# Optimization experiments

Measured on AMD Instinct MI355X. Metric: run time of the kernel, lower is better.

The kernel has to match this reference:

```python
import jax, jax.numpy as jnp
import numpy as np

N, C, H, W = 4, 64, 64, 64
EPS = 1e-5


def setup_inputs() -> dict:
    key = jax.random.key(0)
    ks = jax.random.split(key, 8)
    f = lambda k, s: jax.random.normal(k, s, dtype=jnp.float32)
    return {
        "low_feats": f(ks[0], (N, C, H, W)),
        "heat0": f(ks[1], (N, C, H, W)),
        "heat1": f(ks[2], (N, C, H, W)),
        # f_query: 1x1 conv + BN(gamma,beta) + ReLU
        "Wq": f(ks[3], (C, C)) * 0.05, "bq": jnp.zeros((C,), jnp.float32),
        "gq": jnp.ones((C,), jnp.float32), "betaq": jnp.zeros((C,), jnp.float32),
        # f_key: 1x1 conv + BN + ReLU
        "Wk": f(ks[4], (C, C)) * 0.05, "bk": jnp.zeros((C,), jnp.float32),
        "gk": jnp.ones((C,), jnp.float32), "betak": jnp.zeros((C,), jnp.float32),
        # f_value: plain 1x1 conv
        "Wv": f(ks[5], (C, C)) * 0.05, "bv": jnp.zeros((C,), jnp.float32),
    }


def _conv1x1(x, Wc, bc):
    # [N,C,H,W] -> [N,O,H,W]
    return jnp.einsum("oc,nchw->nohw", Wc, x) + bc[None, :, None, None]


def _conv_bn_relu(x, Wc, bc, g, beta):
    y = _conv1x1(x, Wc, bc)
    mu = y.mean(axis=(0, 2, 3), keepdims=True)      # batch-stat BN (train mode)
    var = y.var(axis=(0, 2, 3), keepdims=True)
    y = (y - mu) * jax.lax.rsqrt(var + EPS)
    y = y * g[None, :, None, None] + beta[None, :, None, None]
    return jax.nn.relu(y)


def reference(low_feats, heat0, heat1, Wq, bq, gq, betaq, Wk, bk, gk, betak, Wv, bv):
    n, c, h, w = low_feats.shape
    hw = h * w
    query = _conv_bn_relu(low_feats, Wq, bq, gq, betaq).reshape(n, c, hw).transpose(0, 2, 1)  # [N,HW,C]
    keym = _conv_bn_relu(low_feats, Wk, bk, gk, betak).reshape(n, c, hw)                      # [N,C,HW]
    value = _conv1x1(low_feats, Wv, bv).reshape(n, c, hw).transpose(0, 2, 1)                  # [N,HW,C]
    sim = jax.nn.softmax(jnp.einsum("nqc,nck->nqk", query, keym), axis=-1)                    # [N,HW,HW]
    # dual gated value paths share the softmax map: sim@vI + sim@vC == sim@(vI+vC)
    gate = (heat0 + heat1).reshape(n, c, hw).transpose(0, 2, 1)                               # [N,HW,C]
    gated_v = gate * value
    ctx = jnp.einsum("nqk,nkc->nqc", sim, gated_v)                                            # [N,HW,C]
    return ctx.transpose(0, 2, 1).reshape(n, c, h, w)
```

## Files before the change

### kernel.cpp

```cpp
#include <hip/hip_runtime.h>

#define NB 4
#define CC 64
#define HW 4096
#define NT (NB*HW)
#define EPSV 1e-5f
#define LOG2E 1.4426950408889634f
#define THRV 8.0f

typedef _Float16 f16;
typedef _Float16 half4 __attribute__((ext_vector_type(4)));
typedef _Float16 half8 __attribute__((ext_vector_type(8)));
typedef float   float4v __attribute__((ext_vector_type(4)));

#define NELEM ((size_t)NB*HW*CC)
#define NSLOT 128

#define PART_OFF 512
#define TEN_OFF  264192

__global__ __launch_bounds__(256)
void conv2_kernel(const float* __restrict__ x,
                  const float* __restrict__ h0, const float* __restrict__ h1,
                  const float* __restrict__ Wq, const float* __restrict__ bq,
                  const float* __restrict__ Wk, const float* __restrict__ bk,
                  const float* __restrict__ Wv, const float* __restrict__ bv,
                  float* __restrict__ ws,
                  f16* __restrict__ q, f16* __restrict__ k, f16* __restrict__ gv)
{
    __shared__ float Wl[3][16*CC];
    __shared__ float xs[CC][128];
    const int t    = threadIdx.x;
    const int n    = blockIdx.y;
    const int z    = blockIdx.z;
    const int px0  = blockIdx.x * 128;
    const int lane = t & 63;
    const int grp  = t >> 6;
    const int ocl  = grp * 4;
    const int oc0  = z*16 + ocl;

    ((float4*)Wl[0])[t] = ((const float4*)(Wq + (size_t)z*16*CC))[t];
    ((float4*)Wl[1])[t] = ((const float4*)(Wk + (size_t)z*16*CC))[t];
    ((float4*)Wl[2])[t] = ((const float4*)(Wv + (size_t)z*16*CC))[t];
    for (int i = t; i < CC*32; i += 256) {
        int ic = i >> 5, c4 = i & 31;
        ((float4*)&xs[ic][0])[c4] =
            ((const float4*)(x + ((size_t)n*CC + ic)*HW + px0))[c4];
    }
    __syncthreads();

    float aq[4][2], ak[4][2], av[4][2];
    #pragma unroll
    for (int j = 0; j < 4; ++j) {
        aq[j][0] = aq[j][1] = bq[oc0+j];
        ak[j][0] = ak[j][1] = bk[oc0+j];
        av[j][0] = av[j][1] = bv[oc0+j];
    }

    for (int ic = 0; ic < CC; ic += 4) {
        float2 xv0 = *(float2*)&xs[ic  ][lane*2];
        float2 xv1 = *(float2*)&xs[ic+1][lane*2];
        float2 xv2 = *(float2*)&xs[ic+2][lane*2];
        float2 xv3 = *(float2*)&xs[ic+3][lane*2];
        #pragma unroll
        for (int j = 0; j < 4; ++j) {
            const int row = (ocl+j)*CC + ic;
            float4 wq = *(const float4*)&Wl[0][row];
            float4 wk = *(const float4*)&Wl[1][row];
            float4 wv = *(const float4*)&Wl[2][row];
            aq[j][0] = fmaf(wq.x,xv0.x, fmaf(wq.y,xv1.x, fmaf(wq.z,xv2.x, fmaf(wq.w,xv3.x, aq[j][0]))));
            aq[j][1] = fmaf(wq.x,xv0.y, fmaf(wq.y,xv1.y, fmaf(wq.z,xv2.y, fmaf(wq.w,xv3.y, aq[j][1]))));
            ak[j][0] = fmaf(wk.x,xv0.x, fmaf(wk.y,xv1.x, fmaf(wk.z,xv2.x, fmaf(wk.w,xv3.x, ak[j][0]))));
            ak[j][1] = fmaf(wk.x,xv0.y, fmaf(wk.y,xv1.y, fmaf(wk.z,xv2.y, fmaf(wk.w,xv3.y, ak[j][1]))));
            av[j][0] = fmaf(wv.x,xv0.x, fmaf(wv.y,xv1.x, fmaf(wv.z,xv2.x, fmaf(wv.w,xv3.x, av[j][0]))));
            av[j][1] = fmaf(wv.x,xv0.y, fmaf(wv.y,xv1.y, fmaf(wv.z,xv2.y, fmaf(wv.w,xv3.y, av[j][1]))));
        }
    }

    const int px = px0 + lane*2;
    const size_t base = ((size_t)n*HW + px)*CC + oc0;
    half4 vq0, vq1, vk0, vk1;
    #pragma unroll
    for (int j = 0; j < 4; ++j) {
        vq0[j] = (f16)aq[j][0]; vq1[j] = (f16)aq[j][1];
        vk0[j] = (f16)ak[j][0]; vk1[j] = (f16)ak[j][1];
    }
    *(half4*)&q[base]      = vq0;  *(half4*)&q[base + CC] = vq1;
    *(half4*)&k[base]      = vk0;  *(half4*)&k[base + CC] = vk1;

    #pragma unroll
    for (int j = 0; j < 4; ++j) {
        size_t gi = ((size_t)n*CC + oc0 + j)*HW + px;
        f16 g0 = (f16)((h0[gi]   + h1[gi]  ) * av[j][0]);
        f16 g1 = (f16)((h0[gi+1] + h1[gi+1]) * av[j][1]);
        gv[gi]   = g0;
        gv[gi+1] = g1;
    }

    float* slot = ws + PART_OFF + (size_t)(n*(HW/128) + blockIdx.x)*256;
    #pragma unroll
    for (int j = 0; j < 4; ++j) {
        float v0 = aq[j][0] + aq[j][1];
        float v1 = aq[j][0]*aq[j][0] + aq[j][1]*aq[j][1];
        float v2 = ak[j][0] + ak[j][1];
        float v3 = ak[j][0]*ak[j][0] + ak[j][1]*ak[j][1];
        #pragma unroll
        for (int off = 32; off > 0; off >>= 1) {
            v0 += __shfl_down(v0, off);
            v1 += __shfl_down(v1, off);
            v2 += __shfl_down(v2, off);
            v3 += __shfl_down(v3, off);
        }
        if (lane == 0) {
            slot[      oc0 + j] = v0;
            slot[ 64 + oc0 + j] = v1;
            slot[128 + oc0 + j] = v2;
            slot[192 + oc0 + j] = v3;
        }
    }
}

__global__ __launch_bounds__(256)
void apply_kernel(f16* __restrict__ q, f16* __restrict__ k,
                  const float* __restrict__ ws,
                  const float* __restrict__ gq, const float* __restrict__ betaq,
                  const float* __restrict__ gk, const float* __restrict__ betak)
{
    __shared__ float tot[128];
    __shared__ float sc[CC], sh[CC];
    const int t = threadIdx.x;
    const int tens = blockIdx.y;

    if (t < 128) {
        const float* base = ws + PART_OFF + tens*128 + t;
        float acc = 0.0f;
        #pragma unroll 8
        for (int s = 0; s < NSLOT; ++s) acc += base[(size_t)s*256];
        tot[t] = acc;
    }
    __syncthreads();
    if (t < 64) {
        float mean = tot[t] * (1.0f / NT);
        float var  = tot[64 + t] * (1.0f / NT) - mean*mean;
        if (tens == 0) {
            float s = gq[t] * rsqrtf(var + EPSV);
            sc[t] = s;  sh[t] = betaq[t] - mean*s;
        } else {
            float s = gk[t] * rsqrtf(var + EPSV);
            sc[t] = s * LOG2E;  sh[t] = (betak[t] - mean*s) * LOG2E;
        }
    }
    __syncthreads();

    f16* p = tens ? k : q;
    const size_t e0 = ((size_t)blockIdx.x * 256 + t) * 16;
    const int c0 = (int)(e0 & 63);

    half8 v0 = *(half8*)&p[e0], v1 = *(half8*)&p[e0 + 8];
    half8 o0, o1;
    #pragma unroll
    for (int j = 0; j < 8; ++j) {
        o0[j] = (f16)fmaxf(fmaf(sc[c0+j],   (float)v0[j], sh[c0+j]),   0.0f);
        o1[j] = (f16)fmaxf(fmaf(sc[c0+8+j], (float)v1[j], sh[c0+8+j]), 0.0f);
    }
    *(half8*)&p[e0]     = o0;
    *(half8*)&p[e0 + 8] = o1;
}

__global__ __launch_bounds__(512, 4)
void attn_kernel(const f16* __restrict__ q, const f16* __restrict__ k,
                 const f16* __restrict__ gv, float* __restrict__ out)
{
    __shared__ alignas(16) char SM[65536];
    f16 (* const Ks)[2][2048]    = reinterpret_cast<f16(*)[2][2048]>(SM);
    f16 (* const GVs)[2][2048]   = reinterpret_cast<f16(*)[2][2048]>(SM + 32768);
    float (* const Obuf)[4][256] = reinterpret_cast<float(*)[4][256]>(SM);
    float (* const MLbuf)[8][16] = reinterpret_cast<float(*)[8][16]>(SM + 32768);

    const int t    = threadIdx.x;
    const int n    = blockIdx.y;
    const int w    = t >> 6;
    const int lane = t & 63;
    const int m16  = lane & 15;
    const int kb   = lane >> 4;
    const int qi   = w >> 2;
    const int si   = w & 3;
    const int q0g  = blockIdx.x * 32 + qi * 16;

    half8 qf0, qf1;
    {
        const size_t qb = ((size_t)n*HW + q0g + m16)*CC + kb*8;
        qf0 = *(const half8*)&q[qb];
        qf1 = *(const half8*)&q[qb + 32];
    }

    const f16* kn  = k  + (size_t)n*HW*CC;
    const f16* gvn = gv + (size_t)n*CC*HW;

    const int rl  = lane >> 3, cl  = lane & 7;
    const int chl = lane >> 2, kcl = lane & 3;
    const int    srcK = rl*CC + cl*8;
    const int    dstK = rl*CC + ((cl ^ rl) * 8);
    const size_t srcG = (size_t)chl*HW + kcl*8;
    const int    dstG = chl*32 + ((kcl ^ (chl & 3)) * 8);

    const int kt00 = si * 1024;

    const int swzk = (m16 & 7) << 3;
    const int swzg = (m16 & 3) << 3;
    const int e0k  = (kb*8)      ^ swzk;
    const int e1k  = (kb*8 + 32) ^ swzk;

    half8 stg[4];

#define STAGE_LOAD(IT) do {                                                   \
    const int kt_ = kt00 + (IT)*32;                                           \
    if (qi == 0) {                                                            \
        const f16* s_ = kn + (size_t)kt_*CC + srcK;                           \
        stg[0] = *(const half8*)(s_);                                         \
        stg[1] = *(const half8*)(s_ +  8*CC);                                 \
        stg[2] = *(const half8*)(s_ + 16*CC);                                 \
        stg[3] = *(const half8*)(s_ + 24*CC);                                 \
    } else {                                                                  \
        const f16* s_ = gvn + srcG + kt_;                                     \
        stg[0] = *(const half8*)(s_);                                         \
        stg[1] = *(const half8*)(s_ + (size_t)16*HW);                         \
        stg[2] = *(const half8*)(s_ + (size_t)32*HW);                         \
        stg[3] = *(const half8*)(s_ + (size_t)48*HW);                         \
    }                                                                         \
} while (0)

#define STAGE_WRITE(BUF) do {                                                 \
    if (qi == 0) {                                                            \
        f16* d_ = &Ks[si][BUF][dstK];                                         \
        *(half8*)(d_)        = stg[0];                                        \
        *(half8*)(d_ +  512) = stg[1];                                        \
        *(half8*)(d_ + 1024) = stg[2];                                        \
        *(half8*)(d_ + 1536) = stg[3];                                        \
    } else {                                                                  \
        f16* d_ = &GVs[si][BUF][dstG];                                        \
        *(half8*)(d_)        = stg[0];                                        \
        *(half8*)(d_ +  512) = stg[1];                                        \
        *(half8*)(d_ + 1024) = stg[2];                                        \
        *(half8*)(d_ + 1536) = stg[3];                                        \
    }                                                                         \
} while (0)

    float4v accO[4];
    #pragma unroll
    for (int ct = 0; ct < 4; ++ct) accO[ct] = (float4v){0.f,0.f,0.f,0.f};
    float accL = 0.0f;
    float mreg = -INFINITY;

#define COMPUTE(CUR) do {                                                     \
    const f16* Kb_ = &Ks[si][CUR][0];                                         \
    const f16* Gb_ = &GVs[si][CUR][0];                                        \
    half8 kh00_ = *(const half8*)&Kb_[ m16*CC       + e0k];                   \
    half8 kh01_ = *(const half8*)&Kb_[ m16*CC       + e1k];                   \
    half8 kh10_ = *(const half8*)&Kb_[(m16+16)*CC   + e0k];                   \
    half8 kh11_ = *(const half8*)&Kb_[(m16+16)*CC   + e1k];                   \
    float4v s0_ = {0.f,0.f,0.f,0.f}, s1_ = {0.f,0.f,0.f,0.f};                 \
    s0_ = __builtin_amdgcn_mfma_f32_16x16x32_f16(kh00_, qf0, s0_, 0,0,0);     \
    s0_ = __builtin_amdgcn_mfma_f32_16x16x32_f16(kh01_, qf1, s0_, 0,0,0);     \
    s1_ = __builtin_amdgcn_mfma_f32_16x16x32_f16(kh10_, qf0, s1_, 0,0,0);     \
    s1_ = __builtin_amdgcn_mfma_f32_16x16x32_f16(kh11_, qf1, s1_, 0,0,0);     \
    float v_ = fmaxf(fmaxf(fmaxf(s0_[0],s0_[1]), fmaxf(s0_[2],s0_[3])),       \
                     fmaxf(fmaxf(s1_[0],s1_[1]), fmaxf(s1_[2],s1_[3])));      \
    v_ = fmaxf(v_, __shfl_xor(v_, 16));                                       \
    v_ = fmaxf(v_, __shfl_xor(v_, 32));                                       \
    if (__any(v_ > mreg + THRV)) {                                            \
        float mn_ = fmaxf(mreg, v_);                                          \
        float al_ = exp2f(mreg - mn_);                                        \
        mreg = mn_;  accL *= al_;                                             \
        _Pragma("unroll") for (int ct_ = 0; ct_ < 4; ++ct_) {                 \
            accO[ct_][0]*=al_; accO[ct_][1]*=al_;                             \
            accO[ct_][2]*=al_; accO[ct_][3]*=al_;                             \
        }                                                                     \
    }                                                                         \
    float p0_=exp2f(s0_[0]-mreg), p1_=exp2f(s0_[1]-mreg);                     \
    float p2_=exp2f(s0_[2]-mreg), p3_=exp2f(s0_[3]-mreg);                     \
    float p4_=exp2f(s1_[0]-mreg), p5_=exp2f(s1_[1]-mreg);                     \
    float p6_=exp2f(s1_[2]-mreg), p7_=exp2f(s1_[3]-mreg);                     \
    accL += ((p0_+p1_)+(p2_+p3_)) + ((p4_+p5_)+(p6_+p7_));                    \
    half4 pfa_, pfb_;                                                         \
    pfa_[0]=(f16)p0_; pfa_[1]=(f16)p1_; pfa_[2]=(f16)p2_; pfa_[3]=(f16)p3_;   \
    pfb_[0]=(f16)p4_; pfb_[1]=(f16)p5_; pfb_[2]=(f16)p6_; pfb_[3]=(f16)p7_;   \
    _Pragma("unroll") for (int ct_ = 0; ct_ < 4; ++ct_) {                     \
        const int gb_ = (ct_*16 + m16)*32;                                    \
        half4 g0_ = *(const half4*)&Gb_[gb_ + ((kb*4)      ^ swzg)];          \
        half4 g1_ = *(const half4*)&Gb_[gb_ + ((kb*4 + 16) ^ swzg)];          \
        float4v o_ = accO[ct_];                                               \
        o_ = __builtin_amdgcn_mfma_f32_16x16x16f16(g0_, pfa_, o_, 0,0,0);     \
        accO[ct_] = __builtin_amdgcn_mfma_f32_16x16x16f16(g1_, pfb_, o_, 0,0,0); \
    }                                                                         \
} while (0)

    STAGE_LOAD(0);
    STAGE_WRITE(0);
    __syncthreads();

    for (int it = 0; it < 31; ++it) {
        const int cur = it & 1;
        STAGE_LOAD(it + 1);
        COMPUTE(cur);
        STAGE_WRITE(cur ^ 1);
        __syncthreads();
    }
    COMPUTE(1);

    float lq = accL;
    lq += __shfl_xor(lq, 16);
    lq += __shfl_xor(lq, 32);
    if (kb == 0) {
        MLbuf[0][w][m16] = mreg;
        MLbuf[1][w][m16] = lq;
    }
    __syncthreads();

    const int wb = qi * 4;
    {
        float M_ = fmaxf(fmaxf(MLbuf[0][wb][m16],   MLbuf[0][wb+1][m16]),
                         fmaxf(MLbuf[0][wb+2][m16], MLbuf[0][wb+3][m16]));
        float f_ = exp2f(mreg - M_);
        #pragma unroll
        for (int ct = 0; ct < 4; ++ct) {
            accO[ct][0]*=f_; accO[ct][1]*=f_; accO[ct][2]*=f_; accO[ct][3]*=f_;
        }
    }
    #pragma unroll
    for (int ct = 0; ct < 4; ++ct)
        ((float4*)&Obuf[w][ct][0])[lane] =
            (float4){accO[ct][0], accO[ct][1], accO[ct][2], accO[ct][3]};
    __syncthreads();

    {
        const int qi2 = w >> 2, ct2 = w & 3, wb2 = qi2 * 4;
        float4 s  = ((float4*)&Obuf[wb2  ][ct2][0])[lane];
        float4 a1 = ((float4*)&Obuf[wb2+1][ct2][0])[lane];
        float4 a2 = ((float4*)&Obuf[wb2+2][ct2][0])[lane];
        float4 a3 = ((float4*)&Obuf[wb2+3][ct2][0])[lane];
        s.x += a1.x + a2.x + a3.x;
        s.y += a1.y + a2.y + a3.y;
        s.z += a1.z + a2.z + a3.z;
        s.w += a1.w + a2.w + a3.w;
        float m0 = MLbuf[0][wb2  ][m16], m1 = MLbuf[0][wb2+1][m16];
        float m2 = MLbuf[0][wb2+2][m16], m3 = MLbuf[0][wb2+3][m16];
        float M_ = fmaxf(fmaxf(m0, m1), fmaxf(m2, m3));
        float L_ = MLbuf[1][wb2  ][m16] * exp2f(m0 - M_)
                 + MLbuf[1][wb2+1][m16] * exp2f(m1 - M_)
                 + MLbuf[1][wb2+2][m16] * exp2f(m2 - M_)
                 + MLbuf[1][wb2+3][m16] * exp2f(m3 - M_);
        const float iv = 1.0f / L_;
        const int chb = ct2*16 + kb*4;
        const int row = blockIdx.x*32 + qi2*16 + m16;
        out[((size_t)n*CC + chb + 0)*HW + row] = s.x * iv;
        out[((size_t)n*CC + chb + 1)*HW + row] = s.y * iv;
        out[((size_t)n*CC + chb + 2)*HW + row] = s.z * iv;
        out[((size_t)n*CC + chb + 3)*HW + row] = s.w * iv;
    }
#undef COMPUTE
#undef STAGE_WRITE
#undef STAGE_LOAD
}

extern "C" void kernel_launch(void* const* d_in, const int* in_sizes, int n_in,
                              void* d_out, int out_size, void* d_ws, size_t ws_size,
                              hipStream_t stream)
{
    const float* low   = (const float*)d_in[0];
    const float* h0    = (const float*)d_in[1];
    const float* h1    = (const float*)d_in[2];
    const float* Wq    = (const float*)d_in[3];
    const float* bq    = (const float*)d_in[4];
    const float* gq    = (const float*)d_in[5];
    const float* betaq = (const float*)d_in[6];
    const float* Wk    = (const float*)d_in[7];
    const float* bk    = (const float*)d_in[8];
    const float* gk    = (const float*)d_in[9];
    const float* betak = (const float*)d_in[10];
    const float* Wv    = (const float*)d_in[11];
    const float* bv    = (const float*)d_in[12];

    float* wsf = (float*)d_ws;
    float* out = (float*)d_out;

    f16* q  = (f16*)((char*)d_ws + TEN_OFF);
    f16* k  = q + NELEM;
    f16* gv = k + NELEM;

    conv2_kernel<<<dim3(HW/128, NB, 4), 256, 0, stream>>>(
        low, h0, h1, Wq, bq, Wk, bk, Wv, bv, wsf, q, k, gv);

    apply_kernel<<<dim3((int)(NELEM/(256*16)), 2), 256, 0, stream>>>(
        q, k, wsf, gq, betaq, gk, betak);

    attn_kernel<<<dim3(HW/32, NB), 512, 0, stream>>>(q, k, gv, out);
}
```

Before: 160.2 us.

## Stage only K in LDS, load gated V directly from global, widen key tile

The attention kernel no longer stages gated-value tiles through shared memory. Each wave now reads its GV MFMA operands straight from global memory as half4 loads, and the whole LDS buffer is given to K tiles. The key tile per iteration doubles from 32 to 64, so there are half as many loop iterations and barriers, and each wave does four score MFMA groups per step. The trade-off is uncoalesced, strided global reads for GV that rely on cache hits, plus more register pressure from the gvf[4][4] array.

```diff
diff --git a/kernel.cpp b/kernel.cpp
--- a/kernel.cpp
+++ b/kernel.cpp
@@ -172,8 +172,7 @@
                  const f16* __restrict__ gv, float* __restrict__ out)
 {
     __shared__ alignas(16) char SM[65536];
-    f16 (* const Ks)[2][2048]    = reinterpret_cast<f16(*)[2][2048]>(SM);
-    f16 (* const GVs)[2][2048]   = reinterpret_cast<f16(*)[2][2048]>(SM + 32768);
+    f16 (* const Ks)[2][4096]    = reinterpret_cast<f16(*)[2][4096]>(SM);
     float (* const Obuf)[4][256] = reinterpret_cast<float(*)[4][256]>(SM);
     float (* const MLbuf)[8][16] = reinterpret_cast<float(*)[8][16]>(SM + 32768);
 
@@ -197,53 +196,33 @@
     const f16* kn  = k  + (size_t)n*HW*CC;
     const f16* gvn = gv + (size_t)n*CC*HW;
 
-    const int rl  = lane >> 3, cl  = lane & 7;
-    const int chl = lane >> 2, kcl = lane & 3;
-    const int    srcK = rl*CC + cl*8;
-    const int    dstK = rl*CC + ((cl ^ rl) * 8);
-    const size_t srcG = (size_t)chl*HW + kcl*8;
-    const int    dstG = chl*32 + ((kcl ^ (chl & 3)) * 8);
+    const int rl    = lane >> 3, cl = lane & 7;
+    const int rbase = qi*32 + rl;
+    const size_t srcK = (size_t)rbase*CC + cl*8;
+    const int    dstK = rbase*CC + ((cl ^ rl) * 8);
 
     const int kt00 = si * 1024;
 
-    const int swzk = (m16 & 7) << 3;
-    const int swzg = (m16 & 3) << 3;
-    const int e0k  = (kb*8)      ^ swzk;
-    const int e1k  = (kb*8 + 32) ^ swzk;
+    const int e0k = ((kb     ^ (m16 & 7)) * 8);
+    const int e1k = (((kb+4) ^ (m16 & 7)) * 8);
 
     half8 stg[4];
+    half4 gvf[4][4];
 
 #define STAGE_LOAD(IT) do {                                                   \
-    const int kt_ = kt00 + (IT)*32;                                           \
-    if (qi == 0) {                                                            \
-        const f16* s_ = kn + (size_t)kt_*CC + srcK;                           \
-        stg[0] = *(const half8*)(s_);                                         \
-        stg[1] = *(const half8*)(s_ +  8*CC);                                 \
-        stg[2] = *(const half8*)(s_ + 16*CC);                                 \
-        stg[3] = *(const half8*)(s_ + 24*CC);                                 \
-    } else {                                                                  \
-        const f16* s_ = gvn + srcG + kt_;                                     \
-        stg[0] = *(const half8*)(s_);                                         \
-        stg[1] = *(const half8*)(s_ + (size_t)16*HW);                         \
-        stg[2] = *(const half8*)(s_ + (size_t)32*HW);                         \
-        stg[3] = *(const half8*)(s_ + (size_t)48*HW);                         \
-    }                                                                         \
+    const f16* s_ = kn + (size_t)(kt00 + (IT)*64)*CC + srcK;                  \
+    stg[0] = *(const half8*)(s_);                                             \
+    stg[1] = *(const half8*)(s_ +  8*CC);                                     \
+    stg[2] = *(const half8*)(s_ + 16*CC);                                     \
+    stg[3] = *(const half8*)(s_ + 24*CC);                                     \
 } while (0)
 
 #define STAGE_WRITE(BUF) do {                                                 \
-    if (qi == 0) {                                                            \
-        f16* d_ = &Ks[si][BUF][dstK];                                         \
-        *(half8*)(d_)        = stg[0];                                        \
-        *(half8*)(d_ +  512) = stg[1];                                        \
-        *(half8*)(d_ + 1024) = stg[2];                                        \
-        *(half8*)(d_ + 1536) = stg[3];                                        \
-    } else {                                                                  \
-        f16* d_ = &GVs[si][BUF][dstG];                                        \
-        *(half8*)(d_)        = stg[0];                                        \
-        *(half8*)(d_ +  512) = stg[1];                                        \
-        *(half8*)(d_ + 1024) = stg[2];                                        \
-        *(half8*)(d_ + 1536) = stg[3];                                        \
-    }                                                                         \
+    f16* d_ = &Ks[si][BUF][dstK];                                             \
+    *(half8*)(d_)        = stg[0];                                            \
+    *(half8*)(d_ +  512) = stg[1];                                            \
+    *(half8*)(d_ + 1024) = stg[2];                                            \
+    *(half8*)(d_ + 1536) = stg[3];                                            \
 } while (0)
 
     float4v accO[4];
@@ -252,20 +231,27 @@
     float accL = 0.0f;
     float mreg = -INFINITY;
 
-#define COMPUTE(CUR) do {                                                     \
+#define COMPUTE(CUR, IT) do {                                                 \
     const f16* Kb_ = &Ks[si][CUR][0];                                         \
-    const f16* Gb_ = &GVs[si][CUR][0];                                        \
-    half8 kh00_ = *(const half8*)&Kb_[ m16*CC       + e0k];                   \
-    half8 kh01_ = *(const half8*)&Kb_[ m16*CC       + e1k];                   \
-    half8 kh10_ = *(const half8*)&Kb_[(m16+16)*CC   + e0k];                   \
-    half8 kh11_ = *(const half8*)&Kb_[(m16+16)*CC   + e1k];                   \
-    float4v s0_ = {0.f,0.f,0.f,0.f}, s1_ = {0.f,0.f,0.f,0.f};                 \
-    s0_ = __builtin_amdgcn_mfma_f32_16x16x32_f16(kh00_, qf0, s0_, 0,0,0);     \
-    s0_ = __builtin_amdgcn_mfma_f32_16x16x32_f16(kh01_, qf1, s0_, 0,0,0);     \
-    s1_ = __builtin_amdgcn_mfma_f32_16x16x32_f16(kh10_, qf0, s1_, 0,0,0);     \
-    s1_ = __builtin_amdgcn_mfma_f32_16x16x32_f16(kh11_, qf1, s1_, 0,0,0);     \
-    float v_ = fmaxf(fmaxf(fmaxf(s0_[0],s0_[1]), fmaxf(s0_[2],s0_[3])),       \
-                     fmaxf(fmaxf(s1_[0],s1_[1]), fmaxf(s1_[2],s1_[3])));      \
+    const int kt_ = kt00 + (IT)*64;                                           \
+    float4v accS[4];                                                          \
+    _Pragma("unroll") for (int kg_ = 0; kg_ < 4; ++kg_) {                     \
+        const int r_ = (kg_*16 + m16)*CC;                                     \
+        half8 kh0_ = *(const half8*)&Kb_[r_ + e0k];                           \
+        half8 kh1_ = *(const half8*)&Kb_[r_ + e1k];                           \
+        float4v s_ = {0.f,0.f,0.f,0.f};                                       \
+        s_ = __builtin_amdgcn_mfma_f32_16x16x32_f16(kh0_, qf0, s_, 0,0,0);    \
+        accS[kg_] = __builtin_amdgcn_mfma_f32_16x16x32_f16(kh1_, qf1, s_, 0,0,0); \
+    }                                                                         \
+    _Pragma("unroll") for (int kg_ = 0; kg_ < 4; ++kg_)                       \
+    _Pragma("unroll") for (int ct_ = 0; ct_ < 4; ++ct_)                       \
+        gvf[kg_][ct_] = *(const half4*)&gvn[(size_t)(ct_*16 + m16)*HW         \
+                                            + kt_ + kg_*16 + kb*4];           \
+    float v_ = fmaxf(fmaxf(fmaxf(accS[0][0],accS[0][1]), fmaxf(accS[0][2],accS[0][3])), \
+                     fmaxf(fmaxf(accS[1][0],accS[1][1]), fmaxf(accS[1][2],accS[1][3]))); \
+    float v2_ = fmaxf(fmaxf(fmaxf(accS[2][0],accS[2][1]), fmaxf(accS[2][2],accS[2][3])), \
+                      fmaxf(fmaxf(accS[3][0],accS[3][1]), fmaxf(accS[3][2],accS[3][3]))); \
+    v_ = fmaxf(v_, v2_);                                                      \
     v_ = fmaxf(v_, __shfl_xor(v_, 16));                                       \
     v_ = fmaxf(v_, __shfl_xor(v_, 32));                                       \
     if (__any(v_ > mreg + THRV)) {                                            \
@@ -277,21 +263,20 @@
             accO[ct_][2]*=al_; accO[ct_][3]*=al_;                             \
         }                                                                     \
     }                                                                         \
-    float p0_=exp2f(s0_[0]-mreg), p1_=exp2f(s0_[1]-mreg);                     \
-    float p2_=exp2f(s0_[2]-mreg), p3_=exp2f(s0_[3]-mreg);                     \
-    float p4_=exp2f(s1_[0]-mreg), p5_=exp2f(s1_[1]-mreg);                     \
-    float p6_=exp2f(s1_[2]-mreg), p7_=exp2f(s1_[3]-mreg);                     \
-    accL += ((p0_+p1_)+(p2_+p3_)) + ((p4_+p5_)+(p6_+p7_));                    \
-    half4 pfa_, pfb_;                                                         \
-    pfa_[0]=(f16)p0_; pfa_[1]=(f16)p1_; pfa_[2]=(f16)p2_; pfa_[3]=(f16)p3_;   \
-    pfb_[0]=(f16)p4_; pfb_[1]=(f16)p5_; pfb_[2]=(f16)p6_; pfb_[3]=(f16)p7_;   \
+    half4 pf_[4];                                                             \
+    _Pragma("unroll") for (int kg_ = 0; kg_ < 4; ++kg_) {                     \
+        float p0_=exp2f(accS[kg_][0]-mreg), p1_=exp2f(accS[kg_][1]-mreg);     \
+        float p2_=exp2f(accS[kg_][2]-mreg), p3_=exp2f(accS[kg_][3]-mreg);     \
+        accL += (p0_+p1_)+(p2_+p3_);                                          \
+        pf_[kg_][0]=(f16)p0_; pf_[kg_][1]=(f16)p1_;                           \
+        pf_[kg_][2]=(f16)p2_; pf_[kg_][3]=(f16)p3_;                           \
+    }                                                                         \
     _Pragma("unroll") for (int ct_ = 0; ct_ < 4; ++ct_) {                     \
-        const int gb_ = (ct_*16 + m16)*32;                                    \
-        half4 g0_ = *(const half4*)&Gb_[gb_ + ((kb*4)      ^ swzg)];          \
-        half4 g1_ = *(const half4*)&Gb_[gb_ + ((kb*4 + 16) ^ swzg)];          \
         float4v o_ = accO[ct_];                                               \
-        o_ = __builtin_amdgcn_mfma_f32_16x16x16f16(g0_, pfa_, o_, 0,0,0);     \
-        accO[ct_] = __builtin_amdgcn_mfma_f32_16x16x16f16(g1_, pfb_, o_, 0,0,0); \
+        o_ = __builtin_amdgcn_mfma_f32_16x16x16f16(gvf[0][ct_], pf_[0], o_, 0,0,0); \
+        o_ = __builtin_amdgcn_mfma_f32_16x16x16f16(gvf[1][ct_], pf_[1], o_, 0,0,0); \
+        o_ = __builtin_amdgcn_mfma_f32_16x16x16f16(gvf[2][ct_], pf_[2], o_, 0,0,0); \
+        accO[ct_] = __builtin_amdgcn_mfma_f32_16x16x16f16(gvf[3][ct_], pf_[3], o_, 0,0,0); \
     }                                                                         \
 } while (0)
 
@@ -299,14 +284,14 @@
     STAGE_WRITE(0);
     __syncthreads();
 
-    for (int it = 0; it < 31; ++it) {
+    for (int it = 0; it < 15; ++it) {
         const int cur = it & 1;
         STAGE_LOAD(it + 1);
-        COMPUTE(cur);
+        COMPUTE(cur, it);
         STAGE_WRITE(cur ^ 1);
         __syncthreads();
     }
-    COMPUTE(1);
+    COMPUTE(1, 15);
 
     float lq = accL;
     lq += __shfl_xor(lq, 16);
```

Measured after the change: 228.5 us. +42.6%, slower.
